# Kernel tuning notes

Hardware: AMD Instinct MI355X
Metric: run time of the kernel (lower is better)

## Reference

```python
import jax, jax.numpy as jnp
import numpy as np

MAX_DIST = 100  # relative_positional_distance


def setup_inputs() -> dict:
    key = jax.random.key(0)
    ks = jax.random.split(key, 6)
    b, s, e, h, d = 4, 2048, 768, 8, 96
    return {
        "x": jax.random.normal(ks[0], (b, s, e), dtype=jnp.float32),
        "w_q": jax.random.normal(ks[1], (h, e, d), dtype=jnp.float32) * 0.02,
        "w_k": jax.random.normal(ks[2], (h, e, d), dtype=jnp.float32) * 0.02,
        "w_v": jax.random.normal(ks[3], (h, e, d), dtype=jnp.float32) * 0.02,
        "w_o": jax.random.normal(ks[4], (h, d, e), dtype=jnp.float32) * 0.02,
        "rel_emb": jax.random.normal(ks[5], (h, 2 * MAX_DIST - 1, d, 1), dtype=jnp.float32) * 0.02,
    }


def _pos_bias(rel_emb, length):
    # Original: gather (h, L, L, d) then sum over d. Equivalent (same math,
    # far less memory): sum over head_dim first, then gather (h, L, L).
    emb_sum = rel_emb[..., 0].sum(axis=-1)  # (h, 2*D-1)
    pos = jnp.arange(length)
    rel = pos[None, :] - pos[:, None]  # (L, L) in [-(L-1), L-1]
    idx = jnp.clip(rel, -(MAX_DIST - 1), MAX_DIST - 1) + MAX_DIST - 1
    return emb_sum[:, idx]  # (h, L, L)


def reference(x, w_q, w_k, w_v, w_o, rel_emb):
    b, s, e = x.shape
    d = w_q.shape[-1]
    q = jnp.einsum("bse,hed->bhsd", x, w_q)
    k = jnp.einsum("bse,hed->bhsd", x, w_k)
    v = jnp.einsum("bse,hed->bhsd", x, w_v)
    scale = d ** -0.5
    logits = jnp.einsum("bhqd,bhkd->bhqk", q, k) * scale  # (b,h,s,s)
    logits = logits + _pos_bias(rel_emb, s)[None]
    attn = jax.nn.softmax(logits, axis=-1)  # dropout p=0 (eval)
    ctx = jnp.einsum("bhqk,bhkd->bhqd", attn, v)
    return jnp.einsum("bhsd,hde->bse", ctx, w_o)
```

## Files before the change

kernel.cpp:

```cpp
#include <hip/hip_runtime.h>

typedef unsigned short u16;
typedef __bf16 v8bf __attribute__((ext_vector_type(8)));
typedef float f32x4 __attribute__((ext_vector_type(4)));
typedef float f32x16 __attribute__((ext_vector_type(16)));

#define LOG2E 1.4426950408889634f

#define GLOAD16(g, l) __builtin_amdgcn_global_load_lds( \
    (const __attribute__((address_space(1))) void*)(g), \
    (__attribute__((address_space(3))) void*)(l), 16, 0, 0)

__device__ __forceinline__ u16 f2b(float x) {
  unsigned u = __builtin_bit_cast(unsigned, x);
  unsigned r = (u + 0x7FFFu + ((u >> 16) & 1u)) >> 16;
  return (u16)r;
}

__device__ __forceinline__ void plswap(unsigned& a, unsigned& b) {
  asm("v_permlane32_swap_b32 %0, %1" : "+v"(a), "+v"(b));
}

union V8U { uint4 u; u16 s[8]; };

__global__ __launch_bounds__(256) void k_cvt_x(const float* __restrict__ x, u16* __restrict__ xb, int nu) {
  int i = blockIdx.x * 256 + threadIdx.x;
  if (i >= nu) return;
  int row = i / 96, cu = i - row * 96;
  const float4* src = (const float4*)(x + (size_t)i * 8);
  float4 a = src[0], c = src[1];
  V8U o;
  o.s[0] = f2b(a.x); o.s[1] = f2b(a.y); o.s[2] = f2b(a.z); o.s[3] = f2b(a.w);
  o.s[4] = f2b(c.x); o.s[5] = f2b(c.y); o.s[6] = f2b(c.z); o.s[7] = f2b(c.w);
  int cus = (cu & ~7) | ((cu & 7) ^ (row & 7));
  *(uint4*)&xb[((size_t)row * 96 + cus) * 8] = o.u;
}

__global__ __launch_bounds__(256) void k_build_wct(const float* __restrict__ wq, const float* __restrict__ wk,
                                                   const float* __restrict__ wv, u16* __restrict__ wct) {
  int t = blockIdx.x * 256 + threadIdx.x;
  if (t >= 2304 * 96) return;
  int c = t / 96, e8 = t - (t / 96) * 96;
  int m = c / 768, rem = c - m * 768;
  int h = rem / 96, d = rem - (rem / 96) * 96;
  const float* src = (m == 0) ? wq : (m == 1) ? wk : wv;
  float sc = (m == 0) ? (0.10206207261596577f * LOG2E) : 1.0f;
  const float* p = src + (size_t)h * 73728 + d;
  V8U o;
  for (int i = 0; i < 8; ++i) o.s[i] = f2b(p[(size_t)(e8 * 8 + i) * 96] * sc);
  int es = (e8 & ~7) | ((e8 & 7) ^ (c & 7));
  *(uint4*)&wct[(size_t)c * 768 + es * 8] = o.u;
}

__global__ __launch_bounds__(256) void k_build_wot(const float* __restrict__ wo, u16* __restrict__ wot) {
  int t = blockIdx.x * 256 + threadIdx.x;
  if (t >= 768 * 96) return;
  int e = t / 96, k8 = t - (t / 96) * 96;
  V8U o;
  for (int i = 0; i < 8; ++i) o.s[i] = f2b(wo[(size_t)(k8 * 8 + i) * 768 + e]);
  int ks = (k8 & ~7) | ((k8 & 7) ^ (e & 7));
  *(uint4*)&wot[(size_t)e * 768 + ks * 8] = o.u;
}

__global__ __launch_bounds__(256) void k_emb(const float* __restrict__ rel, float* __restrict__ emb) {
  int t = blockIdx.x * 256 + threadIdx.x;
  if (t >= 8 * 199) return;
  int h = t / 199, p = t - h * 199;
  const float4* src = (const float4*)(rel + (size_t)(h * 199 + p) * 96);
  float s = 0.f;
  for (int i = 0; i < 24; ++i) { float4 v = src[i]; s += v.x + v.y + v.z + v.w; }
  emb[h * 200 + p] = s * LOG2E;
}

template <int EPI>
__global__ __launch_bounds__(256, 2) void gemm128(const u16* __restrict__ A, const u16* __restrict__ Bm,
                                                  void* __restrict__ Cout) {
  __shared__ alignas(16) u16 Abuf[2][8192];
  __shared__ alignas(16) u16 Bbuf[2][8192];
  const int tid = threadIdx.x, lane = tid & 63, wid = tid >> 6;
  const int g = lane >> 4, r16 = lane & 15;
  const int wr = wid >> 1, wc = wid & 1;
  const int Mbase = blockIdx.y * 128, Nbase = blockIdx.x * 128;
  const int srow = lane >> 3, scq = lane & 7;
  f32x4 acc[4][4];
#pragma unroll
  for (int i = 0; i < 4; ++i)
#pragma unroll
    for (int j = 0; j < 4; ++j) acc[i][j] = (f32x4){0.f, 0.f, 0.f, 0.f};

#define STAGE_G(kt, nb)                                                              \
  {                                                                                  \
    _Pragma("unroll") for (int j = 0; j < 4; ++j) {                                  \
      int blk = 4 * wid + j;                                                         \
      int row = blk * 8 + srow;                                                      \
      GLOAD16(A + (size_t)(Mbase + row) * 768 + (kt)*64 + scq * 8,                   \
              (char*)&Abuf[nb][0] + blk * 1024 + lane * 16);                         \
      GLOAD16(Bm + (size_t)(Nbase + row) * 768 + (kt)*64 + scq * 8,                  \
              (char*)&Bbuf[nb][0] + blk * 1024 + lane * 16);                         \
    }                                                                                \
  }

  STAGE_G(0, 0);
  __syncthreads();
  int cur = 0;
  const int xr = r16 & 7;
  for (int kt = 0; kt < 12; ++kt) {
    if (kt < 11) STAGE_G(kt + 1, cur ^ 1);
    __builtin_amdgcn_s_setprio(1);
#pragma unroll
    for (int ch = 0; ch < 2; ++ch) {
      v8bf af[4], bv[4];
#pragma unroll
      for (int mt = 0; mt < 4; ++mt)
        af[mt] = *(const v8bf*)&Abuf[cur][(64 * wr + 16 * mt + r16) * 64 + (((ch * 4 + g) ^ xr) * 8)];
#pragma unroll
      for (int nt = 0; nt < 4; ++nt)
        bv[nt] = *(const v8bf*)&Bbuf[cur][(64 * wc + 16 * nt + r16) * 64 + (((ch * 4 + g) ^ xr) * 8)];
#pragma unroll
      for (int mt = 0; mt < 4; ++mt)
#pragma unroll
        for (int nt = 0; nt < 4; ++nt)
          acc[mt][nt] = __builtin_amdgcn_mfma_f32_16x16x32_bf16(af[mt], bv[nt], acc[mt][nt], 0, 0, 0);
    }
    __builtin_amdgcn_s_setprio(0);
    __syncthreads();
    cur ^= 1;
  }

  if (EPI == 0) {
    u16* qkv = (u16*)Cout;
#pragma unroll
    for (int mt = 0; mt < 4; ++mt)
#pragma unroll
      for (int nt = 0; nt < 4; ++nt) {
        int col = Nbase + 64 * wc + 16 * nt + r16;
        int m = col / 768, rem = col - m * 768;
        int hh = rem / 96, d = rem - hh * 96;
#pragma unroll
        for (int r = 0; r < 4; ++r) {
          int row = Mbase + 64 * wr + 16 * mt + 4 * g + r;
          int bb = row >> 11, s = row & 2047;
          int bhv = bb * 8 + hh;
          size_t off;
          if (m == 1) {
            int kbv = s >> 6, kblk = (s >> 5) & 1, kl = s & 31;
            int kdv = d >> 4, hi8 = (d >> 3) & 1, e = d & 7;
            off = (size_t)6291456 + ((size_t)bhv * 32 + kbv) * 6144 +
                  (size_t)(kblk * 384 + kdv * 64 + hi8 * 32 + kl) * 8 + e;
          } else {
            off = (size_t)m * 6291456 + ((size_t)bhv * 2048 + s) * 96 + d;
          }
          qkv[off] = f2b(acc[mt][nt][r]);
        }
      }
  } else {
    float* C = (float*)Cout;
#pragma unroll
    for (int mt = 0; mt < 4; ++mt)
#pragma unroll
      for (int nt = 0; nt < 4; ++nt) {
        int col = Nbase + 64 * wc + 16 * nt + r16;
#pragma unroll
        for (int r = 0; r < 4; ++r) {
          int row = Mbase + 64 * wr + 16 * mt + 4 * g + r;
          C[(size_t)row * 768 + col] = acc[mt][nt][r];
        }
      }
  }
#undef STAGE_G
}

__global__ __launch_bounds__(256) void k_packV(const u16* __restrict__ v_ws, u16* __restrict__ vt) {
  __shared__ alignas(16) u16 Vl[64][104];
  int kb = blockIdx.x, bh = blockIdx.y, tid = threadIdx.x;
  const u16* src = v_ws + ((size_t)bh * 2048 + kb * 64) * 96;
#pragma unroll
  for (int j = 0; j < 3; ++j) {
    int u = tid + j * 256;
    int row = u / 12, c8 = u - (u / 12) * 12;
    *(uint4*)&Vl[row][c8 * 8] = *(const uint4*)(src + (size_t)row * 96 + c8 * 8);
  }
  __syncthreads();
  u16* dst = vt + ((size_t)bh * 32 + kb) * 6144;
#pragma unroll
  for (int j = 0; j < 3; ++j) {
    int u = tid + j * 256;
    int dt = u >> 8, ks = (u >> 6) & 3, l = u & 63;
    int dd = dt * 32 + (l & 31), kk = ks * 16 + (l >> 5) * 8;
    V8U o;
#pragma unroll
    for (int e = 0; e < 8; ++e) o.s[e] = Vl[kk + e][dd];
    *(uint4*)&dst[(size_t)u * 8] = o.u;
  }
}

__global__ __launch_bounds__(256, 2) void attn(const u16* __restrict__ q_ws, const u16* __restrict__ kt_ws,
                                               const u16* __restrict__ vt_ws, const float* __restrict__ emb_ws,
                                               u16* __restrict__ ctx) {
  __shared__ alignas(16) u16 Kbuf[2][6144];
  __shared__ alignas(16) u16 Vbuf[2][6144];
  __shared__ float embL[200];
  const int tid = threadIdx.x, lane = tid & 63, wid = tid >> 6;
  const int l31 = lane & 31, hi = lane >> 5;
  const int bh = blockIdx.y, h = bh & 7, b = bh >> 3;
  const int q0 = blockIdx.x * 128;
  for (int i = tid; i < 199; i += 256) embL[i] = emb_ws[h * 200 + i];

  const int q = q0 + wid * 32 + l31;
  const u16* qp = q_ws + ((size_t)bh * 2048 + q) * 96 + hi * 8;
  v8bf qf[6];
#pragma unroll
  for (int kd = 0; kd < 6; ++kd) qf[kd] = *(const v8bf*)(qp + kd * 16);

  const u16* ktp = kt_ws + (size_t)bh * 196608;
  const u16* vtp = vt_ws + (size_t)bh * 196608;

#define STAGE_A(kv, nb)                                                         \
  {                                                                             \
    const u16* ktn = ktp + (size_t)(kv)*6144;                                   \
    const u16* vtn = vtp + (size_t)(kv)*6144;                                   \
    _Pragma("unroll") for (int j = 0; j < 3; ++j) {                             \
      int blk = wid + 4 * j;                                                    \
      GLOAD16(ktn + blk * 512 + lane * 8, (char*)&Kbuf[nb][0] + blk * 1024 + lane * 16); \
      GLOAD16(vtn + blk * 512 + lane * 8, (char*)&Vbuf[nb][0] + blk * 1024 + lane * 16); \
    }                                                                           \
  }

  STAGE_A(0, 0);
  __syncthreads();

  float m_run = -1e30f, l_run = 0.f;
  f32x16 acc[3];
  acc[0] = (f32x16)(0.f); acc[1] = (f32x16)(0.f); acc[2] = (f32x16)(0.f);
  int cur = 0;

  for (int kv = 0; kv < 32; ++kv) {
    const int kb = kv * 64;
    if (kv < 31) STAGE_A(kv + 1, cur ^ 1);
    const u16* Kc = &Kbuf[cur][0];
    const u16* Vc = &Vbuf[cur][0];

    f32x16 sa0 = (f32x16)(0.f), sa1 = (f32x16)(0.f);
    __builtin_amdgcn_s_setprio(1);
#pragma unroll
    for (int kd = 0; kd < 6; ++kd) {
      v8bf k0 = *(const v8bf*)(Kc + kd * 512 + lane * 8);
      v8bf k1 = *(const v8bf*)(Kc + 3072 + kd * 512 + lane * 8);
      sa0 = __builtin_amdgcn_mfma_f32_32x32x16_bf16(k0, qf[kd], sa0, 0, 0, 0);
      sa1 = __builtin_amdgcn_mfma_f32_32x32x16_bf16(k1, qf[kd], sa1, 0, 0, 0);
    }
    __builtin_amdgcn_s_setprio(0);

    const bool nearT = (kb > q0 - 162) && (kb < q0 + 226);
    float bC = 0.f;
    if (nearT) {
      int rb = kb + 99 - q;
#pragma unroll
      for (int r = 0; r < 16; ++r) {
        int kc = (r & 3) + 8 * (r >> 2) + 4 * hi;
        sa0[r] += embL[min(198, max(0, rb + kc))];
        sa1[r] += embL[min(198, max(0, rb + 32 + kc))];
      }
    } else {
      bC = (kb < q0) ? embL[0] : embL[198];
    }

    float pm = -1e30f;
#pragma unroll
    for (int r = 0; r < 16; ++r) pm = fmaxf(pm, fmaxf(sa0[r], sa1[r]));
    pm = fmaxf(pm, __shfl_xor(pm, 32));
    float mb = m_run - bC;

    if (!__all(pm <= mb + 8.f)) {
      float mn = fmaxf(m_run, pm + bC);
      float corr = exp2f(m_run - mn);
      m_run = mn;
      mb = mn - bC;
      l_run *= corr;
#pragma unroll
      for (int r = 0; r < 16; ++r) {
        float cq = __shfl(corr, (r & 3) + 8 * (r >> 2) + 4 * hi);
        acc[0][r] *= cq; acc[1][r] *= cq; acc[2][r] *= cq;
      }
    }

    v8bf pa[2][2];
    float ps = 0.f;
    {
      unsigned u[8];
#pragma unroll
      for (int j = 0; j < 8; ++j) {
        float p0 = exp2f(sa0[2 * j] - mb);
        float p1 = exp2f(sa0[2 * j + 1] - mb);
        ps += p0 + p1;
        asm("v_cvt_pk_bf16_f32 %0, %1, %2" : "=v"(u[j]) : "v"(p0), "v"(p1));
      }
      plswap(u[0], u[2]); plswap(u[1], u[3]); plswap(u[4], u[6]); plswap(u[5], u[7]);
      pa[0][0] = __builtin_bit_cast(v8bf, (uint4){u[0], u[1], u[2], u[3]});
      pa[0][1] = __builtin_bit_cast(v8bf, (uint4){u[4], u[5], u[6], u[7]});
    }
    {
      unsigned u[8];
#pragma unroll
      for (int j = 0; j < 8; ++j) {
        float p0 = exp2f(sa1[2 * j] - mb);
        float p1 = exp2f(sa1[2 * j + 1] - mb);
        ps += p0 + p1;
        asm("v_cvt_pk_bf16_f32 %0, %1, %2" : "=v"(u[j]) : "v"(p0), "v"(p1));
      }
      plswap(u[0], u[2]); plswap(u[1], u[3]); plswap(u[4], u[6]); plswap(u[5], u[7]);
      pa[1][0] = __builtin_bit_cast(v8bf, (uint4){u[0], u[1], u[2], u[3]});
      pa[1][1] = __builtin_bit_cast(v8bf, (uint4){u[4], u[5], u[6], u[7]});
    }
    l_run += ps;

    __builtin_amdgcn_s_setprio(1);
#pragma unroll
    for (int dt = 0; dt < 3; ++dt)
#pragma unroll
      for (int ks = 0; ks < 4; ++ks) {
        v8bf vf = *(const v8bf*)(Vc + dt * 2048 + ks * 512 + lane * 8);
        acc[dt] = __builtin_amdgcn_mfma_f32_32x32x16_bf16(pa[ks >> 1][ks & 1], vf, acc[dt], 0, 0, 0);
      }
    __builtin_amdgcn_s_setprio(0);

    __syncthreads();
    cur ^= 1;
  }
#undef STAGE_A

  float lf = l_run + __shfl_xor(l_run, 32);
#pragma unroll
  for (int r = 0; r < 16; ++r) {
    int qr = (r & 3) + 8 * (r >> 2) + 4 * hi;
    float inv = 1.f / __shfl(lf, qr);
    int s = q0 + wid * 32 + qr;
#pragma unroll
    for (int dt = 0; dt < 3; ++dt) {
      int col = h * 96 + dt * 32 + l31;
      int cu = col >> 3;
      int cus = (cu & ~7) | ((cu & 7) ^ (s & 7));
      ctx[((size_t)b * 2048 + s) * 768 + cus * 8 + (col & 7)] = f2b(acc[dt][r] * inv);
    }
  }
}

extern "C" void kernel_launch(void* const* d_in, const int* in_sizes, int n_in,
                              void* d_out, int out_size, void* d_ws, size_t ws_size,
                              hipStream_t stream) {
  const float* x = (const float*)d_in[0];
  const float* wq = (const float*)d_in[1];
  const float* wk = (const float*)d_in[2];
  const float* wv = (const float*)d_in[3];
  const float* wo = (const float*)d_in[4];
  const float* rel = (const float*)d_in[5];

  char* ws = (char*)d_ws;
  u16* xb = (u16*)(ws + 0);
  u16* wct = (u16*)(ws + 12582912);
  u16* wot = (u16*)(ws + 16121856);
  float* emb = (float*)(ws + 17301504);
  u16* qkv = (u16*)(ws + 17309696);
  u16* ctx = (u16*)(ws + 55058432);

  k_cvt_x<<<3072, 256, 0, stream>>>(x, xb, 786432);
  k_build_wct<<<864, 256, 0, stream>>>(wq, wk, wv, wct);
  k_build_wot<<<288, 256, 0, stream>>>(wo, wot);
  k_emb<<<7, 256, 0, stream>>>(rel, emb);

  dim3 gq(18, 64);
  gemm128<0><<<gq, 256, 0, stream>>>(xb, wct, (void*)qkv);

  u16* vt = xb;
  dim3 gp(32, 32);
  k_packV<<<gp, 256, 0, stream>>>(qkv + 2 * 6291456, vt);

  dim3 ga(16, 32);
  attn<<<ga, 256, 0, stream>>>(qkv, qkv + 6291456, vt, emb, ctx);

  dim3 go(6, 64);
  gemm128<1><<<go, 256, 0, stream>>>(ctx, wot, d_out);
}
```

Measured before the change: 266.6 us.

## Merge prep kernels, fuse V packing into GEMM epilogue, triple-buffer attention

Result: faster. 249.5 us (-6.4%).

```diff
diff --git a/kernel.cpp b/kernel.cpp
--- a/kernel.cpp
+++ b/kernel.cpp
@@ -23,60 +23,57 @@
 
 union V8U { uint4 u; u16 s[8]; };
 
-__global__ __launch_bounds__(256) void k_cvt_x(const float* __restrict__ x, u16* __restrict__ xb, int nu) {
-  int i = blockIdx.x * 256 + threadIdx.x;
-  if (i >= nu) return;
-  int row = i / 96, cu = i - row * 96;
-  const float4* src = (const float4*)(x + (size_t)i * 8);
-  float4 a = src[0], c = src[1];
-  V8U o;
-  o.s[0] = f2b(a.x); o.s[1] = f2b(a.y); o.s[2] = f2b(a.z); o.s[3] = f2b(a.w);
-  o.s[4] = f2b(c.x); o.s[5] = f2b(c.y); o.s[6] = f2b(c.z); o.s[7] = f2b(c.w);
-  int cus = (cu & ~7) | ((cu & 7) ^ (row & 7));
-  *(uint4*)&xb[((size_t)row * 96 + cus) * 8] = o.u;
-}
-
-__global__ __launch_bounds__(256) void k_build_wct(const float* __restrict__ wq, const float* __restrict__ wk,
-                                                   const float* __restrict__ wv, u16* __restrict__ wct) {
-  int t = blockIdx.x * 256 + threadIdx.x;
-  if (t >= 2304 * 96) return;
-  int c = t / 96, e8 = t - (t / 96) * 96;
-  int m = c / 768, rem = c - m * 768;
-  int h = rem / 96, d = rem - (rem / 96) * 96;
-  const float* src = (m == 0) ? wq : (m == 1) ? wk : wv;
-  float sc = (m == 0) ? (0.10206207261596577f * LOG2E) : 1.0f;
-  const float* p = src + (size_t)h * 73728 + d;
-  V8U o;
-  for (int i = 0; i < 8; ++i) o.s[i] = f2b(p[(size_t)(e8 * 8 + i) * 96] * sc);
-  int es = (e8 & ~7) | ((e8 & 7) ^ (c & 7));
-  *(uint4*)&wct[(size_t)c * 768 + es * 8] = o.u;
-}
-
-__global__ __launch_bounds__(256) void k_build_wot(const float* __restrict__ wo, u16* __restrict__ wot) {
-  int t = blockIdx.x * 256 + threadIdx.x;
-  if (t >= 768 * 96) return;
-  int e = t / 96, k8 = t - (t / 96) * 96;
-  V8U o;
-  for (int i = 0; i < 8; ++i) o.s[i] = f2b(wo[(size_t)(k8 * 8 + i) * 768 + e]);
-  int ks = (k8 & ~7) | ((k8 & 7) ^ (e & 7));
-  *(uint4*)&wot[(size_t)e * 768 + ks * 8] = o.u;
-}
-
-__global__ __launch_bounds__(256) void k_emb(const float* __restrict__ rel, float* __restrict__ emb) {
-  int t = blockIdx.x * 256 + threadIdx.x;
-  if (t >= 8 * 199) return;
-  int h = t / 199, p = t - h * 199;
-  const float4* src = (const float4*)(rel + (size_t)(h * 199 + p) * 96);
-  float s = 0.f;
-  for (int i = 0; i < 24; ++i) { float4 v = src[i]; s += v.x + v.y + v.z + v.w; }
-  emb[h * 200 + p] = s * LOG2E;
+__global__ __launch_bounds__(256) void k_prep(const float* __restrict__ x, const float* __restrict__ wq,
+                                              const float* __restrict__ wk, const float* __restrict__ wv,
+                                              const float* __restrict__ wo, const float* __restrict__ rel,
+                                              u16* __restrict__ xb, u16* __restrict__ wct,
+                                              u16* __restrict__ wot, float* __restrict__ emb) {
+  int bx = blockIdx.x;
+  if (bx < 3072) {
+    int i = bx * 256 + threadIdx.x;
+    int row = i / 96, cu = i - row * 96;
+    const float4* src = (const float4*)(x + (size_t)i * 8);
+    float4 a = src[0], c = src[1];
+    V8U o;
+    o.s[0] = f2b(a.x); o.s[1] = f2b(a.y); o.s[2] = f2b(a.z); o.s[3] = f2b(a.w);
+    o.s[4] = f2b(c.x); o.s[5] = f2b(c.y); o.s[6] = f2b(c.z); o.s[7] = f2b(c.w);
+    int cus = (cu & ~7) | ((cu & 7) ^ (row & 7));
+    *(uint4*)&xb[((size_t)row * 96 + cus) * 8] = o.u;
+  } else if (bx < 3936) {
+    int t = (bx - 3072) * 256 + threadIdx.x;
+    int c = t / 96, e8 = t - (t / 96) * 96;
+    int m = c / 768, rem = c - m * 768;
+    int h = rem / 96, d = rem - (rem / 96) * 96;
+    const float* src = (m == 0) ? wq : (m == 1) ? wk : wv;
+    float sc = (m == 0) ? (0.10206207261596577f * LOG2E) : 1.0f;
+    const float* p = src + (size_t)h * 73728 + d;
+    V8U o;
+    for (int i = 0; i < 8; ++i) o.s[i] = f2b(p[(size_t)(e8 * 8 + i) * 96] * sc);
+    int es = (e8 & ~7) | ((e8 & 7) ^ (c & 7));
+    *(uint4*)&wct[(size_t)c * 768 + es * 8] = o.u;
+  } else if (bx < 4224) {
+    int t = (bx - 3936) * 256 + threadIdx.x;
+    int e = t / 96, k8 = t - (t / 96) * 96;
+    V8U o;
+    for (int i = 0; i < 8; ++i) o.s[i] = f2b(wo[(size_t)(k8 * 8 + i) * 768 + e]);
+    int ks = (k8 & ~7) | ((k8 & 7) ^ (e & 7));
+    *(uint4*)&wot[(size_t)e * 768 + ks * 8] = o.u;
+  } else {
+    int t = (bx - 4224) * 256 + threadIdx.x;
+    if (t < 8 * 199) {
+      int h = t / 199, p = t - h * 199;
+      const float4* src = (const float4*)(rel + (size_t)(h * 199 + p) * 96);
+      float s = 0.f;
+      for (int i = 0; i < 24; ++i) { float4 v = src[i]; s += v.x + v.y + v.z + v.w; }
+      emb[h * 200 + p] = s * LOG2E;
+    }
+  }
 }
 
 template <int EPI>
 __global__ __launch_bounds__(256, 2) void gemm128(const u16* __restrict__ A, const u16* __restrict__ Bm,
                                                   void* __restrict__ Cout) {
-  __shared__ alignas(16) u16 Abuf[2][8192];
-  __shared__ alignas(16) u16 Bbuf[2][8192];
+  __shared__ alignas(16) char smem[65536];
   const int tid = threadIdx.x, lane = tid & 63, wid = tid >> 6;
   const int g = lane >> 4, r16 = lane & 15;
   const int wr = wid >> 1, wc = wid & 1;
@@ -94,9 +91,9 @@
       int blk = 4 * wid + j;                                                         \
       int row = blk * 8 + srow;                                                      \
       GLOAD16(A + (size_t)(Mbase + row) * 768 + (kt)*64 + scq * 8,                   \
-              (char*)&Abuf[nb][0] + blk * 1024 + lane * 16);                         \
+              smem + (nb)*16384 + blk * 1024 + lane * 16);                           \
       GLOAD16(Bm + (size_t)(Nbase + row) * 768 + (kt)*64 + scq * 8,                  \
-              (char*)&Bbuf[nb][0] + blk * 1024 + lane * 16);                         \
+              smem + 32768 + (nb)*16384 + blk * 1024 + lane * 16);                   \
     }                                                                                \
   }
 
@@ -112,10 +109,10 @@
       v8bf af[4], bv[4];
 #pragma unroll
       for (int mt = 0; mt < 4; ++mt)
-        af[mt] = *(const v8bf*)&Abuf[cur][(64 * wr + 16 * mt + r16) * 64 + (((ch * 4 + g) ^ xr) * 8)];
+        af[mt] = *(const v8bf*)((u16*)smem + cur * 8192 + (64 * wr + 16 * mt + r16) * 64 + ((ch * 4 + g) ^ xr) * 8);
 #pragma unroll
       for (int nt = 0; nt < 4; ++nt)
-        bv[nt] = *(const v8bf*)&Bbuf[cur][(64 * wc + 16 * nt + r16) * 64 + (((ch * 4 + g) ^ xr) * 8)];
+        bv[nt] = *(const v8bf*)((u16*)(smem + 32768) + cur * 8192 + (64 * wc + 16 * nt + r16) * 64 + ((ch * 4 + g) ^ xr) * 8);
 #pragma unroll
       for (int mt = 0; mt < 4; ++mt)
 #pragma unroll
@@ -126,79 +123,99 @@
     __syncthreads();
     cur ^= 1;
   }
+#undef STAGE_G
+
+  const int colbase = Nbase + 64 * wc;
+  const int sb = Mbase + 64 * wr;
+  const int bI = sb >> 11, sgb = sb & 2047;
 
   if (EPI == 0) {
     u16* qkv = (u16*)Cout;
-#pragma unroll
-    for (int mt = 0; mt < 4; ++mt)
-#pragma unroll
-      for (int nt = 0; nt < 4; ++nt) {
-        int col = Nbase + 64 * wc + 16 * nt + r16;
-        int m = col / 768, rem = col - m * 768;
-        int hh = rem / 96, d = rem - hh * 96;
-#pragma unroll
-        for (int r = 0; r < 4; ++r) {
-          int row = Mbase + 64 * wr + 16 * mt + 4 * g + r;
-          int bb = row >> 11, s = row & 2047;
-          int bhv = bb * 8 + hh;
-          size_t off;
-          if (m == 1) {
-            int kbv = s >> 6, kblk = (s >> 5) & 1, kl = s & 31;
-            int kdv = d >> 4, hi8 = (d >> 3) & 1, e = d & 7;
-            off = (size_t)6291456 + ((size_t)bhv * 32 + kbv) * 6144 +
-                  (size_t)(kblk * 384 + kdv * 64 + hi8 * 32 + kl) * 8 + e;
-          } else {
-            off = (size_t)m * 6291456 + ((size_t)bhv * 2048 + s) * 96 + d;
-          }
-          qkv[off] = f2b(acc[mt][nt][r]);
+    const int m = colbase / 768;
+    u16* W = (u16*)smem + wid * 4608;
+    if (m == 2) {
+#pragma unroll
+      for (int mt = 0; mt < 4; ++mt)
+#pragma unroll
+        for (int nt = 0; nt < 4; ++nt) {
+          int c = 16 * nt + r16;
+#pragma unroll
+          for (int r = 0; r < 4; ++r) W[c * 72 + 16 * mt + 4 * g + r] = f2b(acc[mt][nt][r]);
         }
-      }
+    } else {
+#pragma unroll
+      for (int mt = 0; mt < 4; ++mt)
+#pragma unroll
+        for (int nt = 0; nt < 4; ++nt) {
+          int c = 16 * nt + r16;
+#pragma unroll
+          for (int r = 0; r < 4; ++r) W[(16 * mt + 4 * g + r) * 72 + c] = f2b(acc[mt][nt][r]);
+        }
+    }
+    __builtin_amdgcn_sched_barrier(0);
+    if (m == 0) {
+#pragma unroll
+      for (int j = 0; j < 8; ++j) {
+        int s_l = (lane >> 3) + 8 * j, dchunk = lane & 7;
+        int col = colbase + dchunk * 8;
+        int hh = col / 96, dd = col - hh * 96;
+        size_t off = ((size_t)(bI * 8 + hh) * 2048 + sgb + s_l) * 96 + dd;
+        *(uint4*)&qkv[off] = *(const uint4*)&W[s_l * 72 + dchunk * 8];
+      }
+    } else if (m == 1) {
+      u16* kt_out = qkv + 6291456;
+      const int kbv = sgb >> 6;
+#pragma unroll
+      for (int j = 0; j < 8; ++j) {
+        int kl = lane & 31, hi8 = lane >> 5;
+        int row_l = (j >> 2) * 32 + kl;
+        int d_l = (j & 3) * 16 + hi8 * 8;
+        int rem = colbase + d_l - 768;
+        int hh = rem / 96, dd = rem - hh * 96;
+        size_t off = (((size_t)(bI * 8 + hh) * 32 + kbv) * 768 +
+                      (j >> 2) * 384 + (dd >> 4) * 64 + ((dd >> 3) & 1) * 32 + kl) * 8;
+        *(uint4*)&kt_out[off] = *(const uint4*)&W[row_l * 72 + d_l];
+      }
+    } else {
+      u16* vt_out = qkv + 2 * 6291456;
+      const int kbv = sgb >> 6;
+#pragma unroll
+      for (int j = 0; j < 8; ++j) {
+        int seg = j & 1, ks = j >> 1;
+        int d_l = seg * 32 + (lane & 31);
+        int k_l = ks * 16 + (lane >> 5) * 8;
+        int rem = colbase + d_l - 1536;
+        int hh = rem / 96, dd = rem - hh * 96;
+        size_t off = (((size_t)(bI * 8 + hh) * 32 + kbv) * 768 + (dd >> 5) * 256 + ks * 64 + lane) * 8;
+        *(uint4*)&vt_out[off] = *(const uint4*)&W[d_l * 72 + k_l];
+      }
+    }
   } else {
     float* C = (float*)Cout;
+    float* Wf = (float*)smem + wid * 4096;
 #pragma unroll
     for (int mt = 0; mt < 4; ++mt)
 #pragma unroll
       for (int nt = 0; nt < 4; ++nt) {
-        int col = Nbase + 64 * wc + 16 * nt + r16;
-#pragma unroll
-        for (int r = 0; r < 4; ++r) {
-          int row = Mbase + 64 * wr + 16 * mt + 4 * g + r;
-          C[(size_t)row * 768 + col] = acc[mt][nt][r];
-        }
-      }
-  }
-#undef STAGE_G
-}
-
-__global__ __launch_bounds__(256) void k_packV(const u16* __restrict__ v_ws, u16* __restrict__ vt) {
-  __shared__ alignas(16) u16 Vl[64][104];
-  int kb = blockIdx.x, bh = blockIdx.y, tid = threadIdx.x;
-  const u16* src = v_ws + ((size_t)bh * 2048 + kb * 64) * 96;
-#pragma unroll
-  for (int j = 0; j < 3; ++j) {
-    int u = tid + j * 256;
-    int row = u / 12, c8 = u - (u / 12) * 12;
-    *(uint4*)&Vl[row][c8 * 8] = *(const uint4*)(src + (size_t)row * 96 + c8 * 8);
-  }
-  __syncthreads();
-  u16* dst = vt + ((size_t)bh * 32 + kb) * 6144;
-#pragma unroll
-  for (int j = 0; j < 3; ++j) {
-    int u = tid + j * 256;
-    int dt = u >> 8, ks = (u >> 6) & 3, l = u & 63;
-    int dd = dt * 32 + (l & 31), kk = ks * 16 + (l >> 5) * 8;
-    V8U o;
-#pragma unroll
-    for (int e = 0; e < 8; ++e) o.s[e] = Vl[kk + e][dd];
-    *(uint4*)&dst[(size_t)u * 8] = o.u;
+        int c = 16 * nt + r16;
+#pragma unroll
+        for (int r = 0; r < 4; ++r) Wf[(16 * mt + 4 * g + r) * 64 + c] = acc[mt][nt][r];
+      }
+    __builtin_amdgcn_sched_barrier(0);
+#pragma unroll
+    for (int j = 0; j < 16; ++j) {
+      int s_l = (lane >> 4) + 4 * j, echunk = lane & 15;
+      int row = sb + s_l;
+      *(float4*)&C[(size_t)row * 768 + colbase + echunk * 4] = *(const float4*)&Wf[s_l * 64 + echunk * 4];
+    }
   }
 }
 
 __global__ __launch_bounds__(256, 2) void attn(const u16* __restrict__ q_ws, const u16* __restrict__ kt_ws,
                                                const u16* __restrict__ vt_ws, const float* __restrict__ emb_ws,
                                                u16* __restrict__ ctx) {
-  __shared__ alignas(16) u16 Kbuf[2][6144];
-  __shared__ alignas(16) u16 Vbuf[2][6144];
+  __shared__ alignas(16) u16 Kbuf[3][6144];
+  __shared__ alignas(16) u16 Vbuf[3][6144];
   __shared__ float embL[200];
   const int tid = threadIdx.x, lane = tid & 63, wid = tid >> 6;
   const int l31 = lane & 31, hi = lane >> 5;
@@ -215,18 +232,19 @@
   const u16* ktp = kt_ws + (size_t)bh * 196608;
   const u16* vtp = vt_ws + (size_t)bh * 196608;
 
-#define STAGE_A(kv, nb)                                                         \
-  {                                                                             \
-    const u16* ktn = ktp + (size_t)(kv)*6144;                                   \
-    const u16* vtn = vtp + (size_t)(kv)*6144;                                   \
-    _Pragma("unroll") for (int j = 0; j < 3; ++j) {                             \
-      int blk = wid + 4 * j;                                                    \
-      GLOAD16(ktn + blk * 512 + lane * 8, (char*)&Kbuf[nb][0] + blk * 1024 + lane * 16); \
-      GLOAD16(vtn + blk * 512 + lane * 8, (char*)&Vbuf[nb][0] + blk * 1024 + lane * 16); \
-    }                                                                           \
+#define STAGE_A(kv, nb)                                                                    \
+  {                                                                                        \
+    const u16* ktn = ktp + (size_t)(kv)*6144;                                              \
+    const u16* vtn = vtp + (size_t)(kv)*6144;                                              \
+    _Pragma("unroll") for (int j = 0; j < 3; ++j) {                                        \
+      int blk = wid + 4 * j;                                                               \
+      GLOAD16(ktn + blk * 512 + lane * 8, (char*)&Kbuf[nb][0] + blk * 1024 + lane * 16);   \
+      GLOAD16(vtn + blk * 512 + lane * 8, (char*)&Vbuf[nb][0] + blk * 1024 + lane * 16);   \
+    }                                                                                      \
   }
 
   STAGE_A(0, 0);
+  STAGE_A(1, 1);
   __syncthreads();
 
   float m_run = -1e30f, l_run = 0.f;
@@ -236,7 +254,10 @@
 
   for (int kv = 0; kv < 32; ++kv) {
     const int kb = kv * 64;
-    if (kv < 31) STAGE_A(kv + 1, cur ^ 1);
+    if (kv < 30) {
+      int nb = cur + 2; if (nb >= 3) nb -= 3;
+      STAGE_A(kv + 2, nb);
+    }
     const u16* Kc = &Kbuf[cur][0];
     const u16* Vc = &Vbuf[cur][0];
 
@@ -324,8 +345,16 @@
       }
     __builtin_amdgcn_s_setprio(0);
 
-    __syncthreads();
-    cur ^= 1;
+    if (kv < 30) {
+      asm volatile("s_waitcnt vmcnt(6)" ::: "memory");
+      __builtin_amdgcn_s_barrier();
+      __builtin_amdgcn_sched_barrier(0);
+    } else if (kv == 30) {
+      asm volatile("s_waitcnt vmcnt(0)" ::: "memory");
+      __builtin_amdgcn_s_barrier();
+      __builtin_amdgcn_sched_barrier(0);
+    }
+    cur = (cur == 2) ? 0 : cur + 1;
   }
 #undef STAGE_A
 
@@ -363,20 +392,13 @@
   u16* qkv = (u16*)(ws + 17309696);
   u16* ctx = (u16*)(ws + 55058432);
 
-  k_cvt_x<<<3072, 256, 0, stream>>>(x, xb, 786432);
-  k_build_wct<<<864, 256, 0, stream>>>(wq, wk, wv, wct);
-  k_build_wot<<<288, 256, 0, stream>>>(wo, wot);
-  k_emb<<<7, 256, 0, stream>>>(rel, emb);
+  k_prep<<<4231, 256, 0, stream>>>(x, wq, wk, wv, wo, rel, xb, wct, wot, emb);
 
   dim3 gq(18, 64);
   gemm128<0><<<gq, 256, 0, stream>>>(xb, wct, (void*)qkv);
 
-  u16* vt = xb;
-  dim3 gp(32, 32);
-  k_packV<<<gp, 256, 0, stream>>>(qkv + 2 * 6291456, vt);
-
   dim3 ga(16, 32);
-  attn<<<ga, 256, 0, stream>>>(qkv, qkv + 6291456, vt, emb, ctx);
+  attn<<<ga, 256, 0, stream>>>(qkv, qkv + 6291456, qkv + 2 * 6291456, emb, ctx);
 
   dim3 go(6, 64);
   gemm128<1><<<go, 256, 0, stream>>>(ctx, wot, d_out);
```
